# Kernel tuning notes

Hardware: AMD Instinct MI355X
Metric: run time of the kernel (lower is better)

## Reference

```python
import jax, jax.numpy as jnp
import numpy as np

KS = 3          # kernel size (forced by the view() shape constraint)
STRIDE = 1
PAD = 1
DIL = 1
K = KS * KS     # 9 taps


def _bilinear_sample(x, py, px):
    """x: [B,C,Hin,Win]; py,px: [B,C,K,H,W] float sample coords.
    Zero padding outside bounds (torchvision DeformConv semantics:
    each corner contributes only if it lies inside the image)."""
    B, C, Hin, Win = x.shape
    y0 = jnp.floor(py)
    x0 = jnp.floor(px)
    wy1 = py - y0
    wx1 = px - x0
    wy0 = 1.0 - wy1
    wx0 = 1.0 - wx1
    xf = x.reshape(B, C, Hin * Win)

    def gather(yi, xi):
        valid = (yi >= 0) & (yi <= Hin - 1) & (xi >= 0) & (xi <= Win - 1)
        yc = jnp.clip(yi, 0, Hin - 1).astype(jnp.int32)
        xc = jnp.clip(xi, 0, Win - 1).astype(jnp.int32)
        flat = (yc * Win + xc).reshape(B, C, -1)
        g = jnp.take_along_axis(xf, flat, axis=2).reshape(yi.shape)
        return jnp.where(valid, g, 0.0)

    return (wy0 * wx0 * gather(y0, x0)
            + wy0 * wx1 * gather(y0, x0 + 1)
            + wy1 * wx0 * gather(y0 + 1, x0)
            + wy1 * wx1 * gather(y0 + 1, x0 + 1))


def setup_inputs() -> dict:
    key = jax.random.key(0)
    ks = jax.random.split(key, 5)
    B, C, H, W = 8, 64, 128, 128
    Cout = 64
    return {
        "x": jax.random.normal(ks[0], (B, C, H, W), dtype=jnp.float32),
        # depthwise offset conv: groups=C, out = 18*C -> weight (18C, 1, 3, 3)
        "offset_w": jax.random.normal(ks[1], (2 * K * C, 1, 3, 3), dtype=jnp.float32) * 0.05,
        "offset_b": jax.random.normal(ks[2], (2 * K * C,), dtype=jnp.float32) * 0.05,
        "deform_w": jax.random.normal(ks[3], (Cout, C, KS, KS), dtype=jnp.float32) * 0.05,
        "deform_b": jax.random.normal(ks[4], (Cout,), dtype=jnp.float32) * 0.05,
    }


def reference(x, offset_w, offset_b, deform_w, deform_b):
    B, C, H, W = x.shape
    Cout = deform_w.shape[0]

    # 1) depthwise offset conv (groups = in_channels)
    off = jax.lax.conv_general_dilated(
        x, offset_w, window_strides=(STRIDE, STRIDE),
        padding=((PAD, PAD), (PAD, PAD)), rhs_dilation=(DIL, DIL),
        feature_group_count=C,
        dimension_numbers=("NCHW", "OIHW", "NCHW"))
    off = off + offset_b[None, :, None, None]

    # 2) softmax over the full channel axis (dim=1 in torch)
    off = jax.nn.softmax(off, axis=1)

    # 3) torchvision offset layout: channel 2*(g*K + k) + {0:dy, 1:dx},
    #    deformable_groups = C (per-input-channel offsets)
    off = off.reshape(B, C, K, 2, H, W)
    dy = off[:, :, :, 0]   # [B,C,K,H,W]
    dx = off[:, :, :, 1]

    base_y = (jnp.arange(H, dtype=x.dtype) * STRIDE - PAD)   # [H]
    base_x = (jnp.arange(W, dtype=x.dtype) * STRIDE - PAD)   # [W]
    ky = (jnp.repeat(jnp.arange(KS), KS) * DIL).astype(x.dtype)  # [K]
    kx = (jnp.tile(jnp.arange(KS), KS) * DIL).astype(x.dtype)

    py = base_y[None, None, None, :, None] + ky[None, None, :, None, None] + dy
    px = base_x[None, None, None, None, :] + kx[None, None, :, None, None] + dx

    sampled = _bilinear_sample(x, py, px)                    # [B,C,K,H,W]

    # 4) weighted accumulation over (c_in, kernel tap)
    out = jnp.einsum("bckhw,ock->bohw", sampled, deform_w.reshape(Cout, C, K))
    return out + deform_b[None, :, None, None]
```

## Files before the change

kernel.cpp:

```cpp
#include <hip/hip_runtime.h>

#define B_    8
#define C_    64
#define H_    128
#define W_    128
#define K_    9
#define J_    18
#define COUT_ 64
#define TPX   16
#define CK    576
#define SROW  584

typedef __attribute__((ext_vector_type(8))) short short8;
typedef __attribute__((ext_vector_type(4))) float float4v;

__device__ __forceinline__ unsigned short f2bf(float f) {
    unsigned int u = __float_as_uint(f);
    u = u + 0x7fffu + ((u >> 16) & 1u);
    return (unsigned short)(u >> 16);
}

constexpr int TMAP[9] = {0, 1, 2, 7, 8, 9, 14, 15, 16};

__global__ __launch_bounds__(256)
void nchw_to_nhwc(const float* __restrict__ x, float* __restrict__ xt) {
    __shared__ float tile[64][65];
    const int bid = blockIdx.x;
    const int wt  = bid & 1;
    const int h   = (bid >> 1) & 127;
    const int b   = bid >> 8;
    const int w0  = wt << 6;
    const int q   = threadIdx.x >> 6;
    const int l   = threadIdx.x & 63;
    #pragma unroll
    for (int r = 0; r < 16; r++) {
        const int c = q * 16 + r;
        tile[c][l] = x[((size_t)(b * C_ + c) * H_ + h) * W_ + w0 + l];
    }
    __syncthreads();
    #pragma unroll
    for (int r = 0; r < 16; r++) {
        const int w = q * 16 + r;
        xt[((size_t)(b * H_ + h) * W_ + w0 + w) * C_ + l] = tile[l][w];
    }
}

__global__ __launch_bounds__(256)
void conv_dw_bf16(const float* __restrict__ dw, unsigned short* __restrict__ dwb) {
    const int i = blockIdx.x * 256 + threadIdx.x;
    if (i < CK * COUT_) dwb[i] = f2bf(dw[i]);
}

template<int T>
__device__ __forceinline__ void conv_steps(const unsigned int* __restrict__ owc,
                                           const float (&S)[28], float (&v)[4][J_]) {
    if constexpr (T < 81) {
        const unsigned int pw = owc[T];
        const float wlo = __uint_as_float(pw << 16);
        const float whi = __uint_as_float(pw & 0xffff0000u);
        constexpr int e0 = 2 * T, e1 = 2 * T + 1;
        constexpr int j0 = e0 / 9, p0 = TMAP[e0 % 9];
        constexpr int j1 = e1 / 9, p1 = TMAP[e1 % 9];
        #pragma unroll
        for (int px = 0; px < 4; px++) {
            v[px][j0] = fmaf(wlo, S[p0 + px], v[px][j0]);
            v[px][j1] = fmaf(whi, S[p1 + px], v[px][j1]);
        }
        conv_steps<T + 1>(owc, S, v);
    }
}

template<int I>
__device__ __forceinline__ void finish_px(float (&v)[J_], const float (&S)[28],
                                          unsigned short* __restrict__ sb) {
    float sum = 0.0f;
    #pragma unroll
    for (int j = 0; j < J_; j++) { v[j] = __expf(v[j]); sum += v[j]; }
    #pragma unroll
    for (int off = 32; off >= 1; off >>= 1) sum += __shfl_xor(sum, off, 64);
    const float inv = 1.0f / sum;
    #pragma unroll
    for (int k = 0; k < K_; k++) {
        const float dy = v[2 * k] * inv;
        const float dx = v[2 * k + 1] * inv;
        const int base = TMAP[k] + I;
        const float a  = S[base],     bb = S[base + 1];
        const float c  = S[base + 7], dd = S[base + 8];
        const float top = a + dx * (bb - a);
        const float bot = c + dx * (dd - c);
        sb[k] = f2bf(top + dy * (bot - top));
    }
}

template<bool NHWC, bool PREB>
__global__ __launch_bounds__(256, 3)
void dcn_fused(const float* __restrict__ xsrc,
               const float* __restrict__ ow,
               const float* __restrict__ ob,
               const float* __restrict__ dw,
               const unsigned short* __restrict__ dwb,
               const float* __restrict__ db,
               float* __restrict__ out) {
    __shared__ unsigned int ow_s[C_ * 81];
    __shared__ __align__(16) unsigned short sbuf[TPX * SROW];

    const int tid  = threadIdx.x;
    const int wave = tid >> 6;
    const int lane = tid & 63;

    const int bid = blockIdx.x;
    const int b   = bid >> 10;
    const int rem = bid & 1023;
    const int h   = rem >> 3;
    const int w0  = (rem & 7) << 4;

    const float2* ow2 = (const float2*)ow;
    for (int i = tid; i < C_ * 81; i += 256) {
        float2 f = ow2[i];
        ow_s[i] = (unsigned int)f2bf(f.x) | ((unsigned int)f2bf(f.y) << 16);
    }

    __syncthreads();

    const int wbase = w0 + (wave << 2);
    const unsigned int* owc = ow_s + lane * 81;
    const float2* obp = (const float2*)(ob + lane * J_);

    float S[28];
    #pragma unroll
    for (int r = 0; r < 4; r++) {
        const int y = h - 1 + r;
        const bool yv = (unsigned)y < (unsigned)H_;
        #pragma unroll
        for (int s = 0; s < 7; s++) {
            const int xx = wbase - 1 + s;
            const bool ok = yv && ((unsigned)xx < (unsigned)W_);
            float val;
            if (NHWC) {
                const float* p = xsrc + ((size_t)(b * H_ + (y & 127)) * W_ + (xx & 127)) * C_ + lane;
                val = ok ? *p : 0.0f;
            } else {
                const float* p = xsrc + ((size_t)(b * C_ + lane) * H_ + (y & 127)) * W_ + (xx & 127);
                val = ok ? *p : 0.0f;
            }
            S[r * 7 + s] = val;
        }
    }

    float v[4][J_];
    #pragma unroll
    for (int p = 0; p < 9; p++) {
        const float2 f = obp[p];
        #pragma unroll
        for (int px = 0; px < 4; px++) { v[px][2 * p] = f.x; v[px][2 * p + 1] = f.y; }
    }
    conv_steps<0>(owc, S, v);

    unsigned short* sb = sbuf + (wave << 2) * SROW + lane * K_;
    finish_px<0>(v[0], S, sb);
    finish_px<1>(v[1], S, sb + SROW);
    finish_px<2>(v[2], S, sb + 2 * SROW);
    finish_px<3>(v[3], S, sb + 3 * SROW);

    __syncthreads();

    const int quad = lane >> 4;
    const int o    = (wave << 4) + (lane & 15);
    float4v acc = {0.f, 0.f, 0.f, 0.f};
    const unsigned short* arow = sbuf + (lane & 15) * SROW + quad * 8;
    #pragma unroll
    for (int t = 0; t < 18; t++) {
        short8 afrag = *(const short8*)(arow + t * 32);
        short8 bfrag;
        if (PREB) {
            bfrag = *(const short8*)(dwb + (size_t)o * CK + quad * 8 + t * 32);
        } else {
            const float* brow = dw + (size_t)o * CK + quad * 8 + t * 32;
            float4 b0 = *(const float4*)brow;
            float4 b1 = *(const float4*)(brow + 4);
            union { short8 s8; unsigned short u[8]; } bfu;
            bfu.u[0] = f2bf(b0.x); bfu.u[1] = f2bf(b0.y); bfu.u[2] = f2bf(b0.z); bfu.u[3] = f2bf(b0.w);
            bfu.u[4] = f2bf(b1.x); bfu.u[5] = f2bf(b1.y); bfu.u[6] = f2bf(b1.z); bfu.u[7] = f2bf(b1.w);
            bfrag = bfu.s8;
        }
        acc = __builtin_amdgcn_mfma_f32_16x16x32_bf16(afrag, bfrag, acc, 0, 0, 0);
    }
    const float bias = db[o];
    const int px0 = quad << 2;
    float4 res;
    res.x = acc[0] + bias; res.y = acc[1] + bias; res.z = acc[2] + bias; res.w = acc[3] + bias;
    *(float4*)(out + ((size_t)(b * COUT_ + o) * H_ + h) * W_ + w0 + px0) = res;
}

extern "C" void kernel_launch(void* const* d_in, const int* in_sizes, int n_in,
                              void* d_out, int out_size, void* d_ws, size_t ws_size,
                              hipStream_t stream) {
    (void)in_sizes; (void)n_in; (void)out_size;
    const float* x  = (const float*)d_in[0];
    const float* ow = (const float*)d_in[1];
    const float* ob = (const float*)d_in[2];
    const float* dw = (const float*)d_in[3];
    const float* db = (const float*)d_in[4];
    float* outp = (float*)d_out;

    const size_t xbytes  = (size_t)B_ * C_ * H_ * W_ * sizeof(float);
    const size_t dwbytes = (size_t)CK * COUT_ * sizeof(unsigned short);
    const dim3 grid(B_ * H_ * (W_ / TPX)), blk(256);

    if (ws_size >= xbytes + dwbytes) {
        float* xt = (float*)d_ws;
        unsigned short* dwb = (unsigned short*)((char*)d_ws + xbytes);
        nchw_to_nhwc<<<dim3(B_ * H_ * (W_ / 64)), blk, 0, stream>>>(x, xt);
        conv_dw_bf16<<<dim3((CK * COUT_ + 255) / 256), blk, 0, stream>>>(dw, dwb);
        dcn_fused<true, true><<<grid, blk, 0, stream>>>(xt, ow, ob, dw, dwb, db, outp);
    } else if (ws_size >= xbytes) {
        float* xt = (float*)d_ws;
        nchw_to_nhwc<<<dim3(B_ * H_ * (W_ / 64)), blk, 0, stream>>>(x, xt);
        dcn_fused<true, false><<<grid, blk, 0, stream>>>(xt, ow, ob, dw, nullptr, db, outp);
    } else {
        dcn_fused<false, false><<<grid, blk, 0, stream>>>(x, ow, ob, dw, nullptr, db, outp);
    }
}
```

Before: 206.1 us.

## Stage input halo tile in shared memory as bf16, drop NHWC transpose pass

Removes the separate NCHW-to-NHWC transpose kernel and its workspace round-trip. Each block instead loads its 64-channel by 4-row by 20-column halo from NCHW with float4 loads, converts it to bf16 and stores it in shared memory. The per-lane 4x7 stencil is then read from that tile. Float-to-bf16 conversions also switch to packed pair intrinsics. The trade-offs are extra shared memory, which may lower occupancy, and bf16 rounding of the input samples used for the offset conv and bilinear interpolation.

```diff
diff --git a/kernel.cpp b/kernel.cpp
--- a/kernel.cpp
+++ b/kernel.cpp
@@ -1,4 +1,5 @@
 #include <hip/hip_runtime.h>
+#include <hip/hip_bf16.h>
 
 #define B_    8
 #define C_    64
@@ -10,6 +11,7 @@
 #define TPX   16
 #define CK    576
 #define SROW  584
+#define XTS   84
 
 typedef __attribute__((ext_vector_type(8))) short short8;
 typedef __attribute__((ext_vector_type(4))) float float4v;
@@ -19,31 +21,13 @@
     u = u + 0x7fffu + ((u >> 16) & 1u);
     return (unsigned short)(u >> 16);
 }
+__device__ __forceinline__ unsigned int pk_bf16(float a, float b) {
+    union { __hip_bfloat162 h; unsigned int u; } cvt;
+    cvt.h = __float22bfloat162_rn(float2{a, b});
+    return cvt.u;
+}
 
 constexpr int TMAP[9] = {0, 1, 2, 7, 8, 9, 14, 15, 16};
-
-__global__ __launch_bounds__(256)
-void nchw_to_nhwc(const float* __restrict__ x, float* __restrict__ xt) {
-    __shared__ float tile[64][65];
-    const int bid = blockIdx.x;
-    const int wt  = bid & 1;
-    const int h   = (bid >> 1) & 127;
-    const int b   = bid >> 8;
-    const int w0  = wt << 6;
-    const int q   = threadIdx.x >> 6;
-    const int l   = threadIdx.x & 63;
-    #pragma unroll
-    for (int r = 0; r < 16; r++) {
-        const int c = q * 16 + r;
-        tile[c][l] = x[((size_t)(b * C_ + c) * H_ + h) * W_ + w0 + l];
-    }
-    __syncthreads();
-    #pragma unroll
-    for (int r = 0; r < 16; r++) {
-        const int w = q * 16 + r;
-        xt[((size_t)(b * H_ + h) * W_ + w0 + w) * C_ + l] = tile[l][w];
-    }
-}
 
 __global__ __launch_bounds__(256)
 void conv_dw_bf16(const float* __restrict__ dw, unsigned short* __restrict__ dwb) {
@@ -79,6 +63,7 @@
     #pragma unroll
     for (int off = 32; off >= 1; off >>= 1) sum += __shfl_xor(sum, off, 64);
     const float inv = 1.0f / sum;
+    float smp[K_];
     #pragma unroll
     for (int k = 0; k < K_; k++) {
         const float dy = v[2 * k] * inv;
@@ -88,13 +73,20 @@
         const float c  = S[base + 7], dd = S[base + 8];
         const float top = a + dx * (bb - a);
         const float bot = c + dx * (dd - c);
-        sb[k] = f2bf(top + dy * (bot - top));
-    }
-}
-
-template<bool NHWC, bool PREB>
+        smp[k] = top + dy * (bot - top);
+    }
+    #pragma unroll
+    for (int k = 0; k < 8; k += 2) {
+        const unsigned int q = pk_bf16(smp[k], smp[k + 1]);
+        sb[k]     = (unsigned short)q;
+        sb[k + 1] = (unsigned short)(q >> 16);
+    }
+    sb[8] = f2bf(smp[8]);
+}
+
+template<bool PREB>
 __global__ __launch_bounds__(256, 3)
-void dcn_fused(const float* __restrict__ xsrc,
+void dcn_fused(const float* __restrict__ x,
                const float* __restrict__ ow,
                const float* __restrict__ ob,
                const float* __restrict__ dw,
@@ -103,6 +95,7 @@
                float* __restrict__ out) {
     __shared__ unsigned int ow_s[C_ * 81];
     __shared__ __align__(16) unsigned short sbuf[TPX * SROW];
+    __shared__ __align__(8)  unsigned short xtile[C_ * XTS];
 
     const int tid  = threadIdx.x;
     const int wave = tid >> 6;
@@ -116,35 +109,56 @@
 
     const float2* ow2 = (const float2*)ow;
     for (int i = tid; i < C_ * 81; i += 256) {
-        float2 f = ow2[i];
-        ow_s[i] = (unsigned int)f2bf(f.x) | ((unsigned int)f2bf(f.y) << 16);
+        const float2 f = ow2[i];
+        ow_s[i] = pk_bf16(f.x, f.y);
+    }
+
+    #pragma unroll
+    for (int i = 0; i < 5; i++) {
+        const int flat = i * 256 + tid;
+        const int row  = flat / 5;
+        const int seg  = flat - row * 5;
+        const int c    = row >> 2;
+        const int y    = row & 3;
+        const int gy   = h - 1 + y;
+        const int gx0  = w0 - 1 + (seg << 2);
+        const bool yv  = (unsigned)gy < (unsigned)H_;
+        const float* xr = x + ((size_t)(b * C_ + c) * H_ + (gy & 127)) * W_;
+        float4 f;
+        if (yv && gx0 >= 0 && gx0 + 3 < W_) {
+            f = *(const float4*)(xr + gx0);
+        } else {
+            f.x = (yv && (unsigned)(gx0 + 0) < (unsigned)W_) ? xr[gx0 + 0] : 0.0f;
+            f.y = (yv && (unsigned)(gx0 + 1) < (unsigned)W_) ? xr[gx0 + 1] : 0.0f;
+            f.z = (yv && (unsigned)(gx0 + 2) < (unsigned)W_) ? xr[gx0 + 2] : 0.0f;
+            f.w = (yv && (unsigned)(gx0 + 3) < (unsigned)W_) ? xr[gx0 + 3] : 0.0f;
+        }
+        uint2 pk;
+        pk.x = pk_bf16(f.x, f.y);
+        pk.y = pk_bf16(f.z, f.w);
+        *(uint2*)(xtile + c * XTS + y * 20 + (seg << 2)) = pk;
     }
 
     __syncthreads();
 
-    const int wbase = w0 + (wave << 2);
     const unsigned int* owc = ow_s + lane * 81;
     const float2* obp = (const float2*)(ob + lane * J_);
 
     float S[28];
+    const unsigned short* xtc = xtile + lane * XTS + (wave << 2);
     #pragma unroll
     for (int r = 0; r < 4; r++) {
-        const int y = h - 1 + r;
-        const bool yv = (unsigned)y < (unsigned)H_;
-        #pragma unroll
-        for (int s = 0; s < 7; s++) {
-            const int xx = wbase - 1 + s;
-            const bool ok = yv && ((unsigned)xx < (unsigned)W_);
-            float val;
-            if (NHWC) {
-                const float* p = xsrc + ((size_t)(b * H_ + (y & 127)) * W_ + (xx & 127)) * C_ + lane;
-                val = ok ? *p : 0.0f;
-            } else {
-                const float* p = xsrc + ((size_t)(b * C_ + lane) * H_ + (y & 127)) * W_ + (xx & 127);
-                val = ok ? *p : 0.0f;
-            }
-            S[r * 7 + s] = val;
-        }
+        const unsigned int p01 = *(const unsigned int*)(xtc + r * 20);
+        const unsigned int p23 = *(const unsigned int*)(xtc + r * 20 + 2);
+        const unsigned int p45 = *(const unsigned int*)(xtc + r * 20 + 4);
+        const unsigned short s6 = xtc[r * 20 + 6];
+        S[r * 7 + 0] = __uint_as_float(p01 << 16);
+        S[r * 7 + 1] = __uint_as_float(p01 & 0xffff0000u);
+        S[r * 7 + 2] = __uint_as_float(p23 << 16);
+        S[r * 7 + 3] = __uint_as_float(p23 & 0xffff0000u);
+        S[r * 7 + 4] = __uint_as_float(p45 << 16);
+        S[r * 7 + 5] = __uint_as_float(p45 & 0xffff0000u);
+        S[r * 7 + 6] = __uint_as_float((unsigned int)s6 << 16);
     }
 
     float v[4][J_];
@@ -176,11 +190,11 @@
             bfrag = *(const short8*)(dwb + (size_t)o * CK + quad * 8 + t * 32);
         } else {
             const float* brow = dw + (size_t)o * CK + quad * 8 + t * 32;
-            float4 b0 = *(const float4*)brow;
-            float4 b1 = *(const float4*)(brow + 4);
-            union { short8 s8; unsigned short u[8]; } bfu;
-            bfu.u[0] = f2bf(b0.x); bfu.u[1] = f2bf(b0.y); bfu.u[2] = f2bf(b0.z); bfu.u[3] = f2bf(b0.w);
-            bfu.u[4] = f2bf(b1.x); bfu.u[5] = f2bf(b1.y); bfu.u[6] = f2bf(b1.z); bfu.u[7] = f2bf(b1.w);
+            const float4 b0 = *(const float4*)brow;
+            const float4 b1 = *(const float4*)(brow + 4);
+            union { short8 s8; unsigned int u[4]; } bfu;
+            bfu.u[0] = pk_bf16(b0.x, b0.y); bfu.u[1] = pk_bf16(b0.z, b0.w);
+            bfu.u[2] = pk_bf16(b1.x, b1.y); bfu.u[3] = pk_bf16(b1.z, b1.w);
             bfrag = bfu.s8;
         }
         acc = __builtin_amdgcn_mfma_f32_16x16x32_bf16(afrag, bfrag, acc, 0, 0, 0);
@@ -203,21 +217,14 @@
     const float* db = (const float*)d_in[4];
     float* outp = (float*)d_out;
 
-    const size_t xbytes  = (size_t)B_ * C_ * H_ * W_ * sizeof(float);
     const size_t dwbytes = (size_t)CK * COUT_ * sizeof(unsigned short);
     const dim3 grid(B_ * H_ * (W_ / TPX)), blk(256);
 
-    if (ws_size >= xbytes + dwbytes) {
-        float* xt = (float*)d_ws;
-        unsigned short* dwb = (unsigned short*)((char*)d_ws + xbytes);
-        nchw_to_nhwc<<<dim3(B_ * H_ * (W_ / 64)), blk, 0, stream>>>(x, xt);
+    if (ws_size >= dwbytes) {
+        unsigned short* dwb = (unsigned short*)d_ws;
         conv_dw_bf16<<<dim3((CK * COUT_ + 255) / 256), blk, 0, stream>>>(dw, dwb);
-        dcn_fused<true, true><<<grid, blk, 0, stream>>>(xt, ow, ob, dw, dwb, db, outp);
-    } else if (ws_size >= xbytes) {
-        float* xt = (float*)d_ws;
-        nchw_to_nhwc<<<dim3(B_ * H_ * (W_ / 64)), blk, 0, stream>>>(x, xt);
-        dcn_fused<true, false><<<grid, blk, 0, stream>>>(xt, ow, ob, dw, nullptr, db, outp);
+        dcn_fused<true><<<grid, blk, 0, stream>>>(x, ow, ob, dw, dwb, db, outp);
     } else {
-        dcn_fused<false, false><<<grid, blk, 0, stream>>>(x, ow, ob, dw, nullptr, db, outp);
-    }
-}
+        dcn_fused<false><<<grid, blk, 0, stream>>>(x, ow, ob, dw, nullptr, db, outp);
+    }
+}
```

New measurement: 750.9 us. +264.3%, slower.
